# Optimization experiments

Measured on AMD Instinct MI355X. Metric: run time of the kernel, lower is better.

The kernel has to match this reference:

```python
import jax, jax.numpy as jnp
import numpy as np

B, S, D, H, HID = 64, 1024, 128, 4, 512
HD = D // H  # head dim = 32
EPS = 1e-5


def layer_norm(x, gamma, beta):
    mu = jnp.mean(x, axis=-1, keepdims=True)
    var = jnp.mean(jnp.square(x - mu), axis=-1, keepdims=True)
    return (x - mu) * jax.lax.rsqrt(var + EPS) * gamma + beta


def setup_inputs() -> dict:
    key = jax.random.key(0)
    ks = jax.random.split(key, 16)
    w = lambda k, shp: (jax.random.normal(k, shp, dtype=jnp.float32) * 0.02)
    return {
        "seq": jax.random.normal(ks[0], (B, S, D), dtype=jnp.float32),
        "mask": jnp.ones((B, S, 1), dtype=jnp.float32),
        "Wq": w(ks[1], (D, D)), "bq": jnp.zeros((D,), jnp.float32),
        "Wk": w(ks[2], (D, D)), "bk": jnp.zeros((D,), jnp.float32),
        "Wv": w(ks[3], (D, D)), "bv": jnp.zeros((D,), jnp.float32),
        "g1": jnp.ones((D,), jnp.float32), "be1": jnp.zeros((D,), jnp.float32),
        "g2": jnp.ones((D,), jnp.float32), "be2": jnp.zeros((D,), jnp.float32),
        "W1": w(ks[4], (D, HID)), "bm1": jnp.zeros((HID,), jnp.float32),
        "W2": w(ks[5], (HID, D)), "bm2": jnp.zeros((D,), jnp.float32),
    }


def reference(seq, mask, Wq, bq, Wk, bk, Wv, bv, g1, be1, g2, be2, W1, bm1, W2, bm2):
    # pre-norm queries; keys/values come from the RAW seq (SASRec quirk)
    q_in = layer_norm(seq, g1, be1)           # [B,S,D]
    keys = seq

    Q = (q_in @ Wq + bq).reshape(B, S, H, HD)
    K = (keys @ Wk + bk).reshape(B, S, H, HD)
    V = (keys @ Wv + bv).reshape(B, S, H, HD)

    scores = jnp.einsum("bqhd,bkhd->bhqk", Q, K) / jnp.sqrt(jnp.float32(HD))

    # key padding mask from sign of abs-sum over feature dim
    key_mask = jnp.sign(jnp.sum(jnp.abs(keys), axis=-1))      # [B,S]
    scores = jnp.where(key_mask[:, None, None, :] == 0, -jnp.inf, scores)

    # causal mask
    causal = jnp.tril(jnp.ones((S, S), dtype=bool))
    scores = jnp.where(causal[None, None], scores, -jnp.inf)

    w = jax.nn.softmax(scores, axis=-1)
    w = jnp.nan_to_num(w, nan=0.0, posinf=0.0, neginf=0.0)

    # query padding mask (on the NORMALIZED queries)
    query_mask = jnp.sign(jnp.sum(jnp.abs(q_in), axis=-1))    # [B,S]
    w = w * query_mask[:, None, :, None]
    attentions = w                                            # [B,H,S,S]

    attn_out = jnp.einsum("bhqk,bkhd->bqhd", w, V).reshape(B, S, D)

    x = attn_out + q_in
    x = layer_norm(x, g2, be2)
    h = jax.nn.relu(x @ W1 + bm1)
    y = h @ W2 + bm2 + x
    y = y * mask
    return y, attentions
```

## Files before the change

### kernel.cpp

```cpp
#include <hip/hip_runtime.h>
#include <cstddef>
#include <cstdint>

#define BB 64
#define SS 1024
#define DDIM 128
#define NH 4
#define HDIM 32
#define HIDD 512
#define EPSF 1e-5f
#define SCALEF 0.17677669529663687f
#define LOG2E 1.4426950408889634f

typedef __attribute__((ext_vector_type(8))) short short8;
typedef __attribute__((ext_vector_type(4))) short short4_t;
typedef __attribute__((ext_vector_type(4))) float f32x4;
typedef unsigned short ushort_t;

__device__ __forceinline__ unsigned short f2bf(float f) {
  unsigned u = __builtin_bit_cast(unsigned, f);
  unsigned r = (u + 0x7FFFu + ((u >> 16) & 1u)) >> 16;
  return (unsigned short)r;
}
__device__ __forceinline__ float bf2f(ushort_t h) {
  unsigned u = ((unsigned)h) << 16;
  return __builtin_bit_cast(float, u);
}

__global__ __launch_bounds__(256) void k_cvtw(
    const float* __restrict__ Wq, const float* __restrict__ Wk,
    const float* __restrict__ Wv, const float* __restrict__ W1,
    const float* __restrict__ W2,
    ushort_t* __restrict__ WqT, ushort_t* __restrict__ WkT,
    ushort_t* __restrict__ WvT, ushort_t* __restrict__ W1T,
    ushort_t* __restrict__ W2T) {
  __shared__ float tile[32][33];
  const int bid = blockIdx.x;
  const float* src; ushort_t* dst; int K, N, t0;
  if (bid < 16)       { src = Wq; dst = WqT; K = 128; N = 128; t0 = bid; }
  else if (bid < 32)  { src = Wk; dst = WkT; K = 128; N = 128; t0 = bid - 16; }
  else if (bid < 48)  { src = Wv; dst = WvT; K = 128; N = 128; t0 = bid - 32; }
  else if (bid < 112) { src = W1; dst = W1T; K = 128; N = 512; t0 = bid - 48; }
  else                { src = W2; dst = W2T; K = 512; N = 128; t0 = bid - 112; }
  const int ntile = N >> 5;
  const int k0 = (t0 / ntile) * 32, n0 = (t0 % ntile) * 32;
  const int t = threadIdx.x;
  const int r = t >> 3, c = (t & 7) * 4;
  float4 v = *(const float4*)(src + (size_t)(k0 + r) * N + n0 + c);
  tile[r][c] = v.x; tile[r][c + 1] = v.y; tile[r][c + 2] = v.z; tile[r][c + 3] = v.w;
  __syncthreads();
  ushort4 o;
  o.x = f2bf(tile[c + 0][r]); o.y = f2bf(tile[c + 1][r]);
  o.z = f2bf(tile[c + 2][r]); o.w = f2bf(tile[c + 3][r]);
  *(ushort4*)(dst + (size_t)(n0 + r) * K + k0 + c) = o;
}

__global__ __launch_bounds__(256) void k_ln1(const float* __restrict__ seq,
    const float* __restrict__ g1, const float* __restrict__ be1,
    ushort_t* __restrict__ q_in16, ushort_t* __restrict__ seq16,
    float* __restrict__ qmask, float* __restrict__ kmask) {
  const int t = threadIdx.x;
  const int r = t >> 5, cl = (t & 31) * 4;
  const int row = blockIdx.x * 8 + r;
  const size_t base = (size_t)row * DDIM + cl;
  const f32x4 v4 = *(const f32x4*)(seq + base);
  float sum = v4[0] + v4[1] + v4[2] + v4[3];
  float asum = fabsf(v4[0]) + fabsf(v4[1]) + fabsf(v4[2]) + fabsf(v4[3]);
  #pragma unroll
  for (int o = 1; o < 32; o <<= 1) { sum += __shfl_xor(sum, o); asum += __shfl_xor(asum, o); }
  const float mean = sum * (1.f / DDIM);
  f32x4 d;
  #pragma unroll
  for (int j = 0; j < 4; ++j) d[j] = v4[j] - mean;
  float sq = d[0] * d[0] + d[1] * d[1] + d[2] * d[2] + d[3] * d[3];
  #pragma unroll
  for (int o = 1; o < 32; o <<= 1) sq += __shfl_xor(sq, o);
  const float rsq = rsqrtf(sq * (1.f / DDIM) + EPSF);
  const float4 g4 = *(const float4*)(g1 + cl);
  const float4 b4 = *(const float4*)(be1 + cl);
  float qv[4];
  qv[0] = d[0] * rsq * g4.x + b4.x; qv[1] = d[1] * rsq * g4.y + b4.y;
  qv[2] = d[2] * rsq * g4.z + b4.z; qv[3] = d[3] * rsq * g4.w + b4.w;
  short4_t q4, s4;
  #pragma unroll
  for (int j = 0; j < 4; ++j) { q4[j] = (short)f2bf(qv[j]); s4[j] = (short)f2bf(v4[j]); }
  *(short4_t*)(q_in16 + base) = q4;
  *(short4_t*)(seq16 + base) = s4;
  float aq = fabsf(qv[0]) + fabsf(qv[1]) + fabsf(qv[2]) + fabsf(qv[3]);
  #pragma unroll
  for (int o = 1; o < 32; o <<= 1) aq += __shfl_xor(aq, o);
  if ((t & 31) == 0) {
    kmask[row] = asum > 0.f ? 1.f : 0.f;
    qmask[row] = aq > 0.f ? 1.f : 0.f;
  }
}

__global__ __launch_bounds__(256) void k_qkv_mfma(
    const ushort_t* __restrict__ q_in16, const ushort_t* __restrict__ seq16,
    const ushort_t* __restrict__ WqT, const ushort_t* __restrict__ WkT,
    const ushort_t* __restrict__ WvT,
    const float* __restrict__ bq, const float* __restrict__ bk,
    const float* __restrict__ bv,
    ushort_t* __restrict__ Qo, ushort_t* __restrict__ Ko,
    ushort_t* __restrict__ Vo) {
  const int m = blockIdx.y;
  const int t = threadIdx.x, w = t >> 6, lane = t & 63;
  const int lr = lane & 15, lg = lane >> 4;
  const int row = blockIdx.x * 64 + w * 16;

  if (m == 0) {
    const float sc = SCALEF * LOG2E;
    short8 a[4];
    #pragma unroll
    for (int s = 0; s < 4; ++s)
      a[s] = *(const short8*)(q_in16 + (size_t)(row + lr) * DDIM + s * 32 + lg * 8);
    #pragma unroll
    for (int nt = 0; nt < 8; ++nt) {
      f32x4 acc = {0.f, 0.f, 0.f, 0.f};
      #pragma unroll
      for (int s = 0; s < 4; ++s) {
        short8 b = *(const short8*)(WqT + (size_t)(nt * 16 + lr) * DDIM + s * 32 + lg * 8);
        acc = __builtin_amdgcn_mfma_f32_16x16x32_bf16(b, a[s], acc, 0, 0, 0);
      }
      const int n0 = nt * 16 + lg * 4;
      const float4 bb4 = *(const float4*)(bq + n0);
      short4_t o4;
      o4[0] = (short)f2bf((acc[0] + bb4.x) * sc);
      o4[1] = (short)f2bf((acc[1] + bb4.y) * sc);
      o4[2] = (short)f2bf((acc[2] + bb4.z) * sc);
      o4[3] = (short)f2bf((acc[3] + bb4.w) * sc);
      *(short4_t*)(Qo + (size_t)(row + lr) * DDIM + n0) = o4;
    }
  } else {
    short8 a[4];
    #pragma unroll
    for (int s = 0; s < 4; ++s)
      a[s] = *(const short8*)(seq16 + (size_t)(row + lr) * DDIM + s * 32 + lg * 8);
    #pragma unroll
    for (int nt = 0; nt < 8; ++nt) {
      f32x4 accK = {0.f, 0.f, 0.f, 0.f}, accV = {0.f, 0.f, 0.f, 0.f};
      #pragma unroll
      for (int s = 0; s < 4; ++s) {
        short8 bk8 = *(const short8*)(WkT + (size_t)(nt * 16 + lr) * DDIM + s * 32 + lg * 8);
        short8 bv8 = *(const short8*)(WvT + (size_t)(nt * 16 + lr) * DDIM + s * 32 + lg * 8);
        accK = __builtin_amdgcn_mfma_f32_16x16x32_bf16(bk8, a[s], accK, 0, 0, 0);
        accV = __builtin_amdgcn_mfma_f32_16x16x32_bf16(bv8, a[s], accV, 0, 0, 0);
      }
      const int n0 = nt * 16 + lg * 4;
      const float4 bk4 = *(const float4*)(bk + n0);
      const float4 bv4 = *(const float4*)(bv + n0);
      short4_t k4, v4;
      k4[0] = (short)f2bf(accK[0] + bk4.x); v4[0] = (short)f2bf(accV[0] + bv4.x);
      k4[1] = (short)f2bf(accK[1] + bk4.y); v4[1] = (short)f2bf(accV[1] + bv4.y);
      k4[2] = (short)f2bf(accK[2] + bk4.z); v4[2] = (short)f2bf(accV[2] + bv4.z);
      k4[3] = (short)f2bf(accK[3] + bk4.w); v4[3] = (short)f2bf(accV[3] + bv4.w);
      *(short4_t*)(Ko + (size_t)(row + lr) * DDIM + n0) = k4;
      *(short4_t*)(Vo + (size_t)(row + lr) * DDIM + n0) = v4;
    }
  }
}

__global__ __launch_bounds__(256) void k_attn_mfma(
    const ushort_t* __restrict__ Q, const ushort_t* __restrict__ K,
    const ushort_t* __restrict__ V,
    const float* __restrict__ qmask, const float* __restrict__ kmask,
    float* __restrict__ attn, float* __restrict__ xo) {
  __shared__ __align__(16) ushort_t Ks[2][64 * 40];
  __shared__ __align__(16) ushort_t Vts[2][32 * 72];
  __shared__ __align__(16) ushort_t Wb[4][16 * 88];

  const int t = threadIdx.x;
  const int w = t >> 6, lane = t & 63, lr = lane & 15, lg = lane >> 4;
  const int qi = 15 - (int)blockIdx.x;
  const int q0 = qi << 6;
  const int h = blockIdx.y, b = blockIdx.z;
  const int kend = q0 + 64;
  const int nch = kend >> 6;

  const size_t bS = (size_t)b * SS;
  const ushort_t* Qh = Q + bS * DDIM + h * HDIM;
  const ushort_t* Kh = K + bS * DDIM + h * HDIM;
  const ushort_t* Vh = V + bS * DDIM + h * HDIM;
  float* attn_bh = attn + (size_t)(b * NH + h) * ((size_t)SS * SS);

  {
    const int cnt4 = (SS - kend) >> 2;
    const f32x4 z = {0.f, 0.f, 0.f, 0.f};
    for (int r = w; r < 64; r += 4) {
      float* rowp = attn_bh + (size_t)(q0 + r) * SS + kend;
      for (int c = lane; c < cnt4; c += 64)
        __builtin_nontemporal_store(z, (f32x4*)(rowp + (size_t)c * 4));
    }
  }

  const int qrow = q0 + w * 16 + lr;
  const short8 qf = *(const short8*)(Qh + (size_t)qrow * DDIM + lg * 8);

  const int skr = t >> 2, skc = (t & 3) * 8;

  float lsum = 0.f;
  {
    short8 kreg = *(const short8*)(Kh + (size_t)skr * DDIM + skc);
    *(short8*)(Ks[0] + skr * 40 + skc) = kreg;
    __syncthreads();
    for (int c = 0; c < nch; ++c) {
      const int kc = c << 6;
      const int cur = c & 1;
      if (c + 1 < nch)
        kreg = *(const short8*)(Kh + (size_t)(kc + 64 + skr) * DDIM + skc);
      short8 kf[4];
      #pragma unroll
      for (int T = 0; T < 4; ++T)
        kf[T] = *(const short8*)(Ks[cur] + (T * 16 + lr) * 40 + lg * 8);
      f32x4 acc[4];
      #pragma unroll
      for (int T = 0; T < 4; ++T)
        acc[T] = __builtin_amdgcn_mfma_f32_16x16x32_bf16(kf[T], qf,
                                                         (f32x4){0.f, 0.f, 0.f, 0.f}, 0, 0, 0);
      #pragma unroll
      for (int T = 0; T < 4; ++T) {
        const int k0 = kc + T * 16 + lg * 4;
        const float4 km4 = *(const float4*)(kmask + bS + k0);
        #pragma unroll
        for (int r = 0; r < 4; ++r) {
          const float kmv = r == 0 ? km4.x : (r == 1 ? km4.y : (r == 2 ? km4.z : km4.w));
          const bool dead = (kmv == 0.f) || (k0 + r > qrow);
          lsum += dead ? 0.f : exp2f(acc[T][r]);
        }
      }
      if (c + 1 < nch)
        *(short8*)(Ks[cur ^ 1] + skr * 40 + skc) = kreg;
      __syncthreads();
    }
  }
  float ssum = lsum;
  ssum += __shfl_xor(ssum, 16);
  ssum += __shfl_xor(ssum, 32);
  const float qm = qmask[bS + qrow];
  const float inv = (ssum > 0.f) ? qm / ssum : 0.f;

  ushort_t* myW = &Wb[w][0];
  f32x4 o0 = {0.f, 0.f, 0.f, 0.f}, o1 = {0.f, 0.f, 0.f, 0.f};

  {
    short8 kreg = *(const short8*)(Kh + (size_t)skr * DDIM + skc);
    short8 vreg = *(const short8*)(Vh + (size_t)lane * DDIM + w * 8);
    *(short8*)(Ks[0] + skr * 40 + skc) = kreg;
    #pragma unroll
    for (int j = 0; j < 8; ++j) Vts[0][(w * 8 + j) * 72 + lane] = (ushort_t)vreg[j];
    __syncthreads();
    for (int c = 0; c < nch; ++c) {
      const int kc = c << 6;
      const int cur = c & 1;
      if (c + 1 < nch) {
        kreg = *(const short8*)(Kh + (size_t)(kc + 64 + skr) * DDIM + skc);
        vreg = *(const short8*)(Vh + (size_t)(kc + 64 + lane) * DDIM + w * 8);
      }
      short8 kf[4];
      #pragma unroll
      for (int T = 0; T < 4; ++T)
        kf[T] = *(const short8*)(Ks[cur] + (T * 16 + lr) * 40 + lg * 8);
      f32x4 acc[4];
      #pragma unroll
      for (int T = 0; T < 4; ++T)
        acc[T] = __builtin_amdgcn_mfma_f32_16x16x32_bf16(kf[T], qf,
                                                         (f32x4){0.f, 0.f, 0.f, 0.f}, 0, 0, 0);
      #pragma unroll
      for (int T = 0; T < 4; ++T) {
        const int k0 = kc + T * 16 + lg * 4;
        const float4 km4 = *(const float4*)(kmask + bS + k0);
        f32x4 wv4;
        #pragma unroll
        for (int r = 0; r < 4; ++r) {
          const float kmv = r == 0 ? km4.x : (r == 1 ? km4.y : (r == 2 ? km4.z : km4.w));
          const bool dead = (kmv == 0.f) || (k0 + r > qrow);
          wv4[r] = dead ? 0.f : exp2f(acc[T][r]) * inv;
        }
        __builtin_nontemporal_store(wv4, (f32x4*)(attn_bh + (size_t)qrow * SS + k0));
        short4_t p4;
        p4[0] = (short)f2bf(wv4[0]); p4[1] = (short)f2bf(wv4[1]);
        p4[2] = (short)f2bf(wv4[2]); p4[3] = (short)f2bf(wv4[3]);
        *(short4_t*)(myW + lr * 88 + T * 16 + lg * 4) = p4;
      }
      const short8 af0 = *(const short8*)(myW + lr * 88 + lg * 8);
      const short8 af1 = *(const short8*)(myW + lr * 88 + 32 + lg * 8);
      const short8 vb00 = *(const short8*)(Vts[cur] + (size_t)(lr) * 72 + lg * 8);
      const short8 vb10 = *(const short8*)(Vts[cur] + (size_t)(lr) * 72 + 32 + lg * 8);
      const short8 vb01 = *(const short8*)(Vts[cur] + (size_t)(16 + lr) * 72 + lg * 8);
      const short8 vb11 = *(const short8*)(Vts[cur] + (size_t)(16 + lr) * 72 + 32 + lg * 8);
      o0 = __builtin_amdgcn_mfma_f32_16x16x32_bf16(vb00, af0, o0, 0, 0, 0);
      o0 = __builtin_amdgcn_mfma_f32_16x16x32_bf16(vb10, af1, o0, 0, 0, 0);
      o1 = __builtin_amdgcn_mfma_f32_16x16x32_bf16(vb01, af0, o1, 0, 0, 0);
      o1 = __builtin_amdgcn_mfma_f32_16x16x32_bf16(vb11, af1, o1, 0, 0, 0);
      if (c + 1 < nch) {
        *(short8*)(Ks[cur ^ 1] + skr * 40 + skc) = kreg;
        #pragma unroll
        for (int j = 0; j < 8; ++j) Vts[cur ^ 1][(w * 8 + j) * 72 + lane] = (ushort_t)vreg[j];
      }
      __syncthreads();
    }
  }

  {
    float* op = xo + (bS + qrow) * DDIM + h * HDIM;
    *(f32x4*)(op + lg * 4) = o0;
    *(f32x4*)(op + 16 + lg * 4) = o1;
  }
}

__global__ __launch_bounds__(256) void k_mlp_fused(
    const float* __restrict__ xo, const ushort_t* __restrict__ q_in16,
    const float* __restrict__ g2, const float* __restrict__ be2,
    const ushort_t* __restrict__ W1T, const float* __restrict__ bm1,
    const ushort_t* __restrict__ W2T, const float* __restrict__ bm2,
    const float* __restrict__ mask, float* __restrict__ y) {
  __shared__ __align__(16) ushort_t xls[64 * 136];
  __shared__ __align__(16) ushort_t hs[4][16 * 140];
  const int t = threadIdx.x, w = t >> 6, lane = t & 63;
  const int lr = lane & 15, lg = lane >> 4;
  const int row0 = blockIdx.x * 64;

  {
    const int r = t >> 2, s = t & 3;
    const size_t base = (size_t)(row0 + r) * DDIM + s * 32;
    float v[32];
    float sum = 0.f, sq = 0.f;
    #pragma unroll
    for (int i = 0; i < 4; ++i) {
      const f32x4 x4a = *(const f32x4*)(xo + base + i * 8);
      const f32x4 x4b = *(const f32x4*)(xo + base + i * 8 + 4);
      const short8 q8 = *(const short8*)(q_in16 + base + i * 8);
      #pragma unroll
      for (int j = 0; j < 4; ++j) {
        v[i * 8 + j] = x4a[j] + bf2f((ushort_t)q8[j]);
        v[i * 8 + 4 + j] = x4b[j] + bf2f((ushort_t)q8[4 + j]);
      }
    }
    #pragma unroll
    for (int i = 0; i < 32; ++i) { sum += v[i]; sq += v[i] * v[i]; }
    sum += __shfl_xor(sum, 1); sum += __shfl_xor(sum, 2);
    sq  += __shfl_xor(sq, 1);  sq  += __shfl_xor(sq, 2);
    const float mean = sum * (1.f / DDIM);
    const float var = sq * (1.f / DDIM) - mean * mean;
    const float rsq = rsqrtf(var + EPSF);
    #pragma unroll
    for (int i = 0; i < 8; ++i) {
      const f32x4 g4 = *(const f32x4*)(g2 + s * 32 + i * 4);
      const f32x4 b4 = *(const f32x4*)(be2 + s * 32 + i * 4);
      short4_t o4;
      #pragma unroll
      for (int j = 0; j < 4; ++j)
        o4[j] = (short)f2bf((v[i * 4 + j] - mean) * rsq * g4[j] + b4[j]);
      *(short4_t*)(xls + r * 136 + s * 32 + i * 4) = o4;
    }
  }
  __syncthreads();

  ushort_t* myh = &hs[w][0];
  short8 xa[4];
  #pragma unroll
  for (int s = 0; s < 4; ++s)
    xa[s] = *(const short8*)(xls + (w * 16 + lr) * 136 + s * 32 + lg * 8);

  f32x4 yacc[8];
  #pragma unroll
  for (int i = 0; i < 8; ++i) yacc[i] = (f32x4){0.f, 0.f, 0.f, 0.f};

  for (int c = 0; c < 4; ++c) {
    #pragma unroll
    for (int nt = 0; nt < 8; ++nt) {
      f32x4 acc = {0.f, 0.f, 0.f, 0.f};
      #pragma unroll
      for (int s = 0; s < 4; ++s) {
        short8 b = *(const short8*)(W1T + (size_t)(c * 128 + nt * 16 + lr) * DDIM + s * 32 + lg * 8);
        acc = __builtin_amdgcn_mfma_f32_16x16x32_bf16(b, xa[s], acc, 0, 0, 0);
      }
      const int n0 = nt * 16 + lg * 4;
      const float4 bb4 = *(const float4*)(bm1 + c * 128 + n0);
      short4_t hp;
      hp[0] = (short)f2bf(fmaxf(acc[0] + bb4.x, 0.f));
      hp[1] = (short)f2bf(fmaxf(acc[1] + bb4.y, 0.f));
      hp[2] = (short)f2bf(fmaxf(acc[2] + bb4.z, 0.f));
      hp[3] = (short)f2bf(fmaxf(acc[3] + bb4.w, 0.f));
      *(short4_t*)(myh + lr * 140 + n0) = hp;
    }
    short8 a2[4];
    #pragma unroll
    for (int s = 0; s < 4; ++s)
      a2[s] = *(const short8*)(myh + lr * 140 + s * 32 + lg * 8);
    #pragma unroll
    for (int nt = 0; nt < 8; ++nt) {
      #pragma unroll
      for (int s = 0; s < 4; ++s) {
        short8 b = *(const short8*)(W2T + (size_t)(nt * 16 + lr) * HIDD + c * 128 + s * 32 + lg * 8);
        yacc[nt] = __builtin_amdgcn_mfma_f32_16x16x32_bf16(b, a2[s], yacc[nt], 0, 0, 0);
      }
    }
  }

  const int rr = row0 + w * 16 + lr;
  const float mk = mask[rr];
  #pragma unroll
  for (int nt = 0; nt < 8; ++nt) {
    const int n0 = nt * 16 + lg * 4;
    const float4 bb4 = *(const float4*)(bm2 + n0);
    const ushort4 xv = *(const ushort4*)(xls + (w * 16 + lr) * 136 + n0);
    f32x4 out;
    out[0] = (yacc[nt][0] + bb4.x + bf2f(xv.x)) * mk;
    out[1] = (yacc[nt][1] + bb4.y + bf2f(xv.y)) * mk;
    out[2] = (yacc[nt][2] + bb4.z + bf2f(xv.z)) * mk;
    out[3] = (yacc[nt][3] + bb4.w + bf2f(xv.w)) * mk;
    *(f32x4*)(y + (size_t)rr * DDIM + n0) = out;
  }
}

extern "C" void kernel_launch(void* const* d_in, const int* in_sizes, int n_in,
                              void* d_out, int out_size, void* d_ws, size_t ws_size,
                              hipStream_t stream) {
  const float* seq  = (const float*)d_in[0];
  const float* mask = (const float*)d_in[1];
  const float* Wq = (const float*)d_in[2];
  const float* bq = (const float*)d_in[3];
  const float* Wk = (const float*)d_in[4];
  const float* bk = (const float*)d_in[5];
  const float* Wv = (const float*)d_in[6];
  const float* bv = (const float*)d_in[7];
  const float* g1 = (const float*)d_in[8];
  const float* be1 = (const float*)d_in[9];
  const float* g2 = (const float*)d_in[10];
  const float* be2 = (const float*)d_in[11];
  const float* W1 = (const float*)d_in[12];
  const float* bm1 = (const float*)d_in[13];
  const float* W2 = (const float*)d_in[14];
  const float* bm2 = (const float*)d_in[15];

  float* ws   = (float*)d_ws;
  float* xb   = ws;
  float* qmk  = ws + 8388608;
  float* kmk  = ws + 8454144;
  ushort_t* sbase  = (ushort_t*)(ws + 8519680);
  ushort_t* Qb     = sbase;
  ushort_t* Kb     = sbase + 8388608;
  ushort_t* Vb     = sbase + 16777216;
  ushort_t* q_in16 = sbase + 25165824;
  ushort_t* seq16  = sbase + 33554432;
  ushort_t* WqT    = sbase + 41943040;
  ushort_t* WkT    = WqT + 16384;
  ushort_t* WvT    = WkT + 16384;
  ushort_t* W1T    = WvT + 16384;
  ushort_t* W2T    = W1T + 65536;

  float* y    = (float*)d_out;
  float* attn = y + 8388608;

  hipLaunchKernelGGL(k_cvtw, dim3(176), dim3(256), 0, stream,
                     Wq, Wk, Wv, W1, W2, WqT, WkT, WvT, W1T, W2T);
  hipLaunchKernelGGL(k_ln1, dim3(BB * SS / 8), dim3(256), 0, stream,
                     seq, g1, be1, q_in16, seq16, qmk, kmk);
  hipLaunchKernelGGL(k_qkv_mfma, dim3(1024, 2), dim3(256), 0, stream,
                     q_in16, seq16, WqT, WkT, WvT, bq, bk, bv, Qb, Kb, Vb);
  hipLaunchKernelGGL(k_attn_mfma, dim3(16, NH, BB), dim3(256), 0, stream,
                     Qb, Kb, Vb, qmk, kmk, attn, xb);
  hipLaunchKernelGGL(k_mlp_fused, dim3(1024), dim3(256), 0, stream,
                     xb, q_in16, g2, be2, W1T, bm1, W2T, bm2, mask, y);
}
```

Measured before the change: 573.7 us.

## Single-pass attention with deferred normalization via bf16 scratch and separate normalize kernel

Removes the first QK^T pass that only computed softmax denominators. Unnormalized bf16 weights go to the upper half of each attention output row, and the PV result is scaled by the inverse sum at the end. A new kernel reads the bf16 scratch, scales it by the stored inverse and writes the final fp32 row including zeros. This trades one full QK^T/exp pass for an extra read of the bf16 half-row and one more launch. Normalized weights are now rounded to bf16 before scaling, which changes precision slightly.

```diff
diff --git a/kernel.cpp b/kernel.cpp
--- a/kernel.cpp
+++ b/kernel.cpp
@@ -164,7 +164,8 @@
     const ushort_t* __restrict__ Q, const ushort_t* __restrict__ K,
     const ushort_t* __restrict__ V,
     const float* __restrict__ qmask, const float* __restrict__ kmask,
-    float* __restrict__ attn, float* __restrict__ xo) {
+    float* __restrict__ attn, float* __restrict__ xo,
+    float* __restrict__ invb) {
   __shared__ __align__(16) ushort_t Ks[2][64 * 40];
   __shared__ __align__(16) ushort_t Vts[2][32 * 72];
   __shared__ __align__(16) ushort_t Wb[4][16 * 88];
@@ -183,64 +184,15 @@
   const ushort_t* Vh = V + bS * DDIM + h * HDIM;
   float* attn_bh = attn + (size_t)(b * NH + h) * ((size_t)SS * SS);
 
-  {
-    const int cnt4 = (SS - kend) >> 2;
-    const f32x4 z = {0.f, 0.f, 0.f, 0.f};
-    for (int r = w; r < 64; r += 4) {
-      float* rowp = attn_bh + (size_t)(q0 + r) * SS + kend;
-      for (int c = lane; c < cnt4; c += 64)
-        __builtin_nontemporal_store(z, (f32x4*)(rowp + (size_t)c * 4));
-    }
-  }
-
   const int qrow = q0 + w * 16 + lr;
   const short8 qf = *(const short8*)(Qh + (size_t)qrow * DDIM + lg * 8);
+  ushort_t* rowu = (ushort_t*)(attn_bh + (size_t)qrow * SS) + 1024;
 
   const int skr = t >> 2, skc = (t & 3) * 8;
-
-  float lsum = 0.f;
-  {
-    short8 kreg = *(const short8*)(Kh + (size_t)skr * DDIM + skc);
-    *(short8*)(Ks[0] + skr * 40 + skc) = kreg;
-    __syncthreads();
-    for (int c = 0; c < nch; ++c) {
-      const int kc = c << 6;
-      const int cur = c & 1;
-      if (c + 1 < nch)
-        kreg = *(const short8*)(Kh + (size_t)(kc + 64 + skr) * DDIM + skc);
-      short8 kf[4];
-      #pragma unroll
-      for (int T = 0; T < 4; ++T)
-        kf[T] = *(const short8*)(Ks[cur] + (T * 16 + lr) * 40 + lg * 8);
-      f32x4 acc[4];
-      #pragma unroll
-      for (int T = 0; T < 4; ++T)
-        acc[T] = __builtin_amdgcn_mfma_f32_16x16x32_bf16(kf[T], qf,
-                                                         (f32x4){0.f, 0.f, 0.f, 0.f}, 0, 0, 0);
-      #pragma unroll
-      for (int T = 0; T < 4; ++T) {
-        const int k0 = kc + T * 16 + lg * 4;
-        const float4 km4 = *(const float4*)(kmask + bS + k0);
-        #pragma unroll
-        for (int r = 0; r < 4; ++r) {
-          const float kmv = r == 0 ? km4.x : (r == 1 ? km4.y : (r == 2 ? km4.z : km4.w));
-          const bool dead = (kmv == 0.f) || (k0 + r > qrow);
-          lsum += dead ? 0.f : exp2f(acc[T][r]);
-        }
-      }
-      if (c + 1 < nch)
-        *(short8*)(Ks[cur ^ 1] + skr * 40 + skc) = kreg;
-      __syncthreads();
-    }
-  }
-  float ssum = lsum;
-  ssum += __shfl_xor(ssum, 16);
-  ssum += __shfl_xor(ssum, 32);
-  const float qm = qmask[bS + qrow];
-  const float inv = (ssum > 0.f) ? qm / ssum : 0.f;
 
   ushort_t* myW = &Wb[w][0];
   f32x4 o0 = {0.f, 0.f, 0.f, 0.f}, o1 = {0.f, 0.f, 0.f, 0.f};
+  float lsum = 0.f;
 
   {
     short8 kreg = *(const short8*)(Kh + (size_t)skr * DDIM + skc);
@@ -274,13 +226,14 @@
         for (int r = 0; r < 4; ++r) {
           const float kmv = r == 0 ? km4.x : (r == 1 ? km4.y : (r == 2 ? km4.z : km4.w));
           const bool dead = (kmv == 0.f) || (k0 + r > qrow);
-          wv4[r] = dead ? 0.f : exp2f(acc[T][r]) * inv;
+          wv4[r] = dead ? 0.f : exp2f(acc[T][r]);
         }
-        __builtin_nontemporal_store(wv4, (f32x4*)(attn_bh + (size_t)qrow * SS + k0));
+        lsum += wv4[0] + wv4[1] + wv4[2] + wv4[3];
         short4_t p4;
         p4[0] = (short)f2bf(wv4[0]); p4[1] = (short)f2bf(wv4[1]);
         p4[2] = (short)f2bf(wv4[2]); p4[3] = (short)f2bf(wv4[3]);
         *(short4_t*)(myW + lr * 88 + T * 16 + lg * 4) = p4;
+        __builtin_nontemporal_store(p4, (short4_t*)(rowu + k0));
       }
       const short8 af0 = *(const short8*)(myW + lr * 88 + lg * 8);
       const short8 af1 = *(const short8*)(myW + lr * 88 + 32 + lg * 8);
@@ -301,10 +254,53 @@
     }
   }
 
+  float ssum = lsum;
+  ssum += __shfl_xor(ssum, 16);
+  ssum += __shfl_xor(ssum, 32);
+  const float qm = qmask[bS + qrow];
+  const float inv = (ssum > 0.f) ? qm / ssum : 0.f;
+  if (lane < 16) invb[(((size_t)b * NH + h) << 10) + qrow] = inv;
+
   {
+    f32x4 r0, r1;
+    #pragma unroll
+    for (int r = 0; r < 4; ++r) { r0[r] = o0[r] * inv; r1[r] = o1[r] * inv; }
     float* op = xo + (bS + qrow) * DDIM + h * HDIM;
-    *(f32x4*)(op + lg * 4) = o0;
-    *(f32x4*)(op + 16 + lg * 4) = o1;
+    *(f32x4*)(op + lg * 4) = r0;
+    *(f32x4*)(op + 16 + lg * 4) = r1;
+  }
+}
+
+__global__ __launch_bounds__(256) void k_attn_norm(
+    const float* __restrict__ invb, float* __restrict__ attn) {
+  const int t = threadIdx.x, w = t >> 6, lane = t & 63;
+  const int q = blockIdx.x * 4 + w;
+  const int h = blockIdx.y, b = blockIdx.z;
+  float* row = attn + (size_t)(b * NH + h) * ((size_t)SS * SS) + (size_t)q * SS;
+  const ushort_t* rowu = (const ushort_t*)row + 1024;
+  const int kend = ((q >> 6) + 1) << 6;
+  const float inv = invb[(((size_t)b * NH + h) << 10) + q];
+
+  short4_t s4[4];
+  #pragma unroll
+  for (int i = 0; i < 4; ++i)
+    if (i * 256 < kend)
+      s4[i] = *(const short4_t*)(rowu + i * 256 + lane * 4);
+  asm volatile("s_waitcnt vmcnt(0)" ::: "memory");
+
+  #pragma unroll
+  for (int i = 0; i < 4; ++i) {
+    const int k0 = i * 256 + lane * 4;
+    f32x4 out;
+    if (k0 < kend) {
+      out[0] = bf2f((ushort_t)s4[i][0]) * inv;
+      out[1] = bf2f((ushort_t)s4[i][1]) * inv;
+      out[2] = bf2f((ushort_t)s4[i][2]) * inv;
+      out[3] = bf2f((ushort_t)s4[i][3]) * inv;
+    } else {
+      out = (f32x4){0.f, 0.f, 0.f, 0.f};
+    }
+    __builtin_nontemporal_store(out, (f32x4*)(row + k0));
   }
 }
 
@@ -438,7 +434,8 @@
   float* xb   = ws;
   float* qmk  = ws + 8388608;
   float* kmk  = ws + 8454144;
-  ushort_t* sbase  = (ushort_t*)(ws + 8519680);
+  float* invb = ws + 8519680;
+  ushort_t* sbase  = (ushort_t*)(ws + 8781824);
   ushort_t* Qb     = sbase;
   ushort_t* Kb     = sbase + 8388608;
   ushort_t* Vb     = sbase + 16777216;
@@ -460,7 +457,9 @@
   hipLaunchKernelGGL(k_qkv_mfma, dim3(1024, 2), dim3(256), 0, stream,
                      q_in16, seq16, WqT, WkT, WvT, bq, bk, bv, Qb, Kb, Vb);
   hipLaunchKernelGGL(k_attn_mfma, dim3(16, NH, BB), dim3(256), 0, stream,
-                     Qb, Kb, Vb, qmk, kmk, attn, xb);
+                     Qb, Kb, Vb, qmk, kmk, attn, xb, invb);
+  hipLaunchKernelGGL(k_attn_norm, dim3(SS / 4, NH, BB), dim3(256), 0, stream,
+                     invb, attn);
   hipLaunchKernelGGL(k_mlp_fused, dim3(1024), dim3(256), 0, stream,
                      xb, q_in16, g2, be2, W1T, bm1, W2T, bm2, mask, y);
 }
```

Result: slower. 871.9 us (+52.0%).
